# Optimization experiments

Measured on AMD Instinct MI355X. Metric: run time of the kernel, lower is better.

The kernel has to match this reference:

```python
import jax, jax.numpy as jnp
import numpy as np

B, S, HID = 2, 2048, 2048
H, D = 16, 128  # heads, head_dim == kernel_hidden_size
GATE_NORM = 16.0
CLAMP_MIN = -50.0


def gla(q, k, v, gk):
    # fused_recurrent_gla: S_t = diag(exp(gk_t)) S_{t-1} + k_t^T v_t; o_t = (q_t*scale) @ S_t
    # q,k,v,gk: [B,H,S,D]
    scale = D ** -0.5
    qs = jnp.moveaxis(q, 2, 0) * scale  # [S,B,H,D]
    ks = jnp.moveaxis(k, 2, 0)
    vs = jnp.moveaxis(v, 2, 0)
    gs = jnp.moveaxis(gk, 2, 0)

    def step(state, xs):
        q_t, k_t, v_t, g_t = xs  # each [B,H,D]
        state = state * jnp.exp(g_t)[..., None] + k_t[..., None] * v_t[..., None, :]
        o_t = jnp.einsum('bhk,bhkv->bhv', q_t, state)
        return state, o_t

    init = jnp.zeros((q.shape[0], H, D, D), q.dtype)
    _, out = jax.lax.scan(step, init, (qs, ks, vs, gs))
    return jnp.moveaxis(out, 0, 2)  # [B,H,S,D]


def setup_inputs() -> dict:
    key = jax.random.key(0)
    ks = jax.random.split(key, 8)
    std = 0.02
    hidden_states = jax.random.normal(ks[0], (B, S, HID), jnp.float32)
    Wq = jax.random.normal(ks[1], (HID, HID), jnp.float32) * std
    Wk = jax.random.normal(ks[2], (HID, HID), jnp.float32) * std
    Wv = jax.random.normal(ks[3], (HID, HID), jnp.float32) * std
    Wo = jax.random.normal(ks[4], (HID, HID), jnp.float32) * std
    Wg1 = jnp.eye(HID, dtype=jnp.float32)  # nn.init.eye_
    bg1 = jnp.zeros((HID,), jnp.float32)
    Wg2 = jnp.eye(HID, dtype=jnp.float32)
    bg2 = jnp.zeros((HID,), jnp.float32)
    alpha_list = jax.random.uniform(ks[5], (2,), jnp.float32)
    return dict(hidden_states=hidden_states, Wq=Wq, Wk=Wk, Wv=Wv, Wo=Wo,
                Wg1=Wg1, bg1=bg1, Wg2=Wg2, bg2=bg2, alpha_list=alpha_list)


def reference(hidden_states, Wq, Wk, Wv, Wo, Wg1, bg1, Wg2, bg2, alpha_list):
    b, s, _ = hidden_states.shape

    def split_heads(x):  # [b,s,hid] -> [b,h,s,d]
        return x.reshape(b, s, H, D).transpose(0, 2, 1, 3)

    q = split_heads(hidden_states @ Wq.T)
    k = split_heads(hidden_states @ Wk.T)
    v = split_heads(hidden_states @ Wv.T)

    def gate(Wg, bg):
        g = split_heads(hidden_states @ Wg.T + bg)
        g = jax.nn.log_sigmoid(g) / GATE_NORM
        return jnp.maximum(g, CLAMP_MIN)

    gk = gate(Wg1, bg1)
    gk2 = gate(Wg2, bg2)

    o1 = gla(q, k, v, gk)
    o2 = gla(q, k, v, gk2)

    a = jax.nn.softmax(alpha_list)
    attn = a[0] * o1 + a[1] * o2  # [b,h,s,d]
    attn = attn.transpose(0, 2, 1, 3).reshape(b, s, HID)
    return attn @ Wo.T
```

## Files before the change

### kernel.cpp

```cpp
#include <hip/hip_runtime.h>
#include <cstdint>
#include <cstddef>


#define BB     2
#define SEQ    2048
#define HIDN   2048
#define NH     16
#define DD     128
#define CHUNK  64
#define NCHUNK (SEQ / CHUNK)
#define NBH    (BB * NH)
#define NELC   8388608
#define WELC   4194304
static constexpr float QSCALE = 0.08838834764831845f;

typedef __bf16 bf16_t;
typedef _Float16 half_t;
typedef short  short8 __attribute__((ext_vector_type(8)));
typedef float  f32x4  __attribute__((ext_vector_type(4)));

__device__ __forceinline__ float bf2f(short u) {
  return (float)__builtin_bit_cast(bf16_t, u);
}
__device__ __forceinline__ short f2bf(float f) {
  return __builtin_bit_cast(short, (bf16_t)f);
}
__device__ __forceinline__ float hf2f(short u) {
  return (float)__builtin_bit_cast(half_t, u);
}
__device__ __forceinline__ short f2hf(float f) {
  return __builtin_bit_cast(short, (half_t)f);
}

__device__ __forceinline__ void gload_lds16(const void* g, void* l) {
  __builtin_amdgcn_global_load_lds(
      (__attribute__((address_space(1))) unsigned int*)g,
      (__attribute__((address_space(3))) unsigned int*)l, 16, 0, 0);
}

#define VMW6 asm volatile("s_waitcnt vmcnt(6)" ::: "memory")
#define VMW0 asm volatile("s_waitcnt vmcnt(0)" ::: "memory")
#define LGKM0 asm volatile("s_waitcnt lgkmcnt(0)" ::: "memory")
#define SBAR __builtin_amdgcn_s_barrier()


#define STG_A(buf, kt, pair)                                                \
  {                                                                         \
    const size_t ko = (size_t)(kt) * 64;                                    \
    gload_lds16(Ag + (size_t)((pair) * 64) * HIDN + ko,                     \
                (void*)&As[buf][((pair) * 64 + wave * 8) * 64]);            \
    gload_lds16(Ag + (size_t)((pair) * 64 + 128) * HIDN + ko,               \
                (void*)&As[buf][((pair) * 64 + 128 + wave * 8) * 64]);      \
  }

#define STG_B(buf, kt, half)                                                \
  {                                                                         \
    gload_lds16(Bg + (size_t)((half) * 64) * HIDN + (size_t)(kt) * 64,      \
                (void*)&Bs[buf][((half) * 64 + wave * 8) * 64]);            \
  }

#define LDA_PH(mh, rb)                                                      \
  {                                                                         \
    _Pragma("unroll") for (int f = 0; f < 4; f++) {                         \
      const int row = wm * 128 + (mh) * 64 + f * 16 + l16;                  \
      ar[f][0] = *(const short8*)&As[rb][row * 64 + ((qd ^ ro) << 3)];      \
      ar[f][1] =                                                            \
          *(const short8*)&As[rb][row * 64 + (((4 + qd) ^ ro) << 3)];       \
    }                                                                       \
  }

#define LDB_PH(rb)                                                          \
  {                                                                         \
    _Pragma("unroll") for (int g = 0; g < 2; g++) {                         \
      const int col = wn * 32 + g * 16 + l16;                               \
      br[g][0] = *(const short8*)&Bs[rb][col * 64 + ((qd ^ ro) << 3)];      \
      br[g][1] =                                                            \
          *(const short8*)&Bs[rb][col * 64 + (((4 + qd) ^ ro) << 3)];       \
    }                                                                       \
  }

#define MFMA_PH(mh)                                                         \
  {                                                                         \
    __builtin_amdgcn_s_setprio(1);                                          \
    _Pragma("unroll") for (int ks = 0; ks < 2; ks++)                        \
    _Pragma("unroll") for (int f = 0; f < 4; f++)                           \
    _Pragma("unroll") for (int g = 0; g < 2; g++)                           \
      acc[(mh) * 4 + f][g] = __builtin_amdgcn_mfma_f32_16x16x32_bf16(       \
          ar[f][ks], br[g][ks], acc[(mh) * 4 + f][g], 0, 0, 0);             \
    __builtin_amdgcn_s_setprio(0);                                          \
  }

__device__ __forceinline__ void gemm256(const bf16_t* __restrict__ A,
                                        const bf16_t* __restrict__ Bw,
                                        const float*  __restrict__ bias,
                                        bf16_t* __restrict__ outb,
                                        float*  __restrict__ outf, int epi) {
  __shared__ short As[3][256 * 64];
  __shared__ short Bs[3][128 * 64];
  const int tm   = blockIdx.x * 256;
  const int tn   = blockIdx.y * 128;
  const int tid  = threadIdx.x;
  const int wave = tid >> 6;
  const int lane = tid & 63;
  const int wm   = wave >> 2;
  const int wn   = wave & 3;
  const int qd   = lane >> 4;
  const int l16  = lane & 15;
  const int ro   = l16 & 7;
  const int gc   = (lane & 7) ^ (lane >> 3);

  const short* Ag =
      (const short*)A + (size_t)(tm + wave * 8 + (lane >> 3)) * HIDN + gc * 8;
  const short* Bg =
      (const short*)Bw + (size_t)(tn + wave * 8 + (lane >> 3)) * HIDN + gc * 8;

  f32x4 acc[8][2];
#pragma unroll
  for (int i = 0; i < 8; i++)
#pragma unroll
    for (int j = 0; j < 2; j++) acc[i][j] = (f32x4){0.f, 0.f, 0.f, 0.f};
  short8 ar[4][2], br[2][2];

  STG_A(0, 0, 0); STG_B(0, 0, 0); STG_B(0, 0, 1); STG_A(0, 0, 1);
  STG_A(1, 1, 0); STG_B(1, 1, 0); STG_B(1, 1, 1); STG_A(1, 1, 1);
  VMW6;
  SBAR;

  int rd = 0, st = 2;
  for (int t = 0; t < 32; t++) {
    LDA_PH(0, rd);
    LDB_PH(rd);
    if (t < 30) { STG_A(st, t + 2, 0); STG_B(st, t + 2, 0); }
    SBAR;
    LGKM0;
    MFMA_PH(0);
    SBAR;
    LDA_PH(1, rd);
    if (t < 30) { STG_B(st, t + 2, 1); STG_A(st, t + 2, 1); }
    SBAR;
    LGKM0;
    MFMA_PH(1);
    if (t < 30) { VMW6; }
    else if (t == 30) { VMW0; }
    SBAR;
    rd = (rd == 2) ? 0 : rd + 1;
    st = (st == 2) ? 0 : st + 1;
  }

#pragma unroll
  for (int i = 0; i < 8; i++)
#pragma unroll
    for (int j = 0; j < 2; j++)
#pragma unroll
      for (int r = 0; r < 4; r++) {
        const int row =
            tm + wm * 128 + (i >> 2) * 64 + (i & 3) * 16 + qd * 4 + r;
        const int col = tn + wn * 32 + j * 16 + l16;
        float v = acc[i][j][r];
        if (epi == 1) {
          v += bias[col];
          const float ls = fminf(v, 0.f) - log1pf(__expf(-fabsf(v)));
          v = fmaxf(ls * 0.0625f, -50.f);
        }
        if (epi == 2) outf[(size_t)row * HIDN + col] = v;
        else          outb[(size_t)row * HIDN + col] = (bf16_t)v;
      }
}

__global__ __launch_bounds__(512, 2) void k_gemm_proj(
    const bf16_t* __restrict__ Xb,
    const bf16_t* __restrict__ W0, const bf16_t* __restrict__ W1,
    const bf16_t* __restrict__ W2, const bf16_t* __restrict__ W3,
    const bf16_t* __restrict__ W4,
    const float* __restrict__ bg1, const float* __restrict__ bg2,
    bf16_t* __restrict__ Qb, bf16_t* __restrict__ Kb, bf16_t* __restrict__ Vb,
    bf16_t* __restrict__ G1b, bf16_t* __restrict__ G2b) {
  const int z = blockIdx.z;
  const bf16_t* Ws[5] = {W0, W1, W2, W3, W4};
  bf16_t* Os[5] = {Qb, Kb, Vb, G1b, G2b};
  const float* bias = (z == 3) ? bg1 : ((z == 4) ? bg2 : nullptr);
  gemm256(Xb, Ws[z], bias, Os[z], nullptr, (z >= 3) ? 1 : 0);
}

__global__ __launch_bounds__(512, 2) void k_gemm_out(
    const bf16_t* __restrict__ attnB, const bf16_t* __restrict__ Wob,
    float* __restrict__ out) {
  gemm256(attnB, Wob, nullptr, nullptr, out, 2);
}

__global__ __launch_bounds__(256) void k_cvt_all(
    const float* __restrict__ hid, const float* __restrict__ wq,
    const float* __restrict__ wk, const float* __restrict__ wv,
    const float* __restrict__ wg1, const float* __restrict__ wg2,
    const float* __restrict__ wo, bf16_t* __restrict__ Xb,
    bf16_t* __restrict__ Wd, bf16_t* __restrict__ Wcur,
    bf16_t* __restrict__ WoB) {
  const int y = blockIdx.y;
  const float* srcs[7] = {hid, wq, wk, wv, wg1, wg2, wo};
  bf16_t* dsts[7] = {Xb, Wd, Wd + WELC, Wd + 2 * WELC, Wd + 3 * WELC, Wcur,
                     WoB};
  const int n = (y == 0) ? NELC : WELC;
  const float* src = srcs[y];
  bf16_t* dst = dsts[y];
  const int idx = (blockIdx.x * 256 + threadIdx.x) * 4;
  if (idx < n) {
    const float4 f = *(const float4*)(src + idx);
    dst[idx + 0] = (bf16_t)f.x; dst[idx + 1] = (bf16_t)f.y;
    dst[idx + 2] = (bf16_t)f.z; dst[idx + 3] = (bf16_t)f.w;
  }
}

__global__ __launch_bounds__(256) void k_zero(float* __restrict__ out) {
  out[(size_t)blockIdx.x * 256 + threadIdx.x] = 0.f;
}

__global__ __launch_bounds__(64) void k_gc(bf16_t* __restrict__ G1b,
                                           bf16_t* __restrict__ G2b,
                                           float* __restrict__ Btot) {
  const int n = blockIdx.x, b = blockIdx.y >> 2, slab = blockIdx.y & 3;
  const int e = blockIdx.z;
  short* P = (short*)(e ? G2b : G1b);
  const int d0 = slab * 512 + threadIdx.x * 8;
  const size_t base = ((size_t)(b * SEQ + n * CHUNK)) * HIDN + d0;
  float c[8] = {0.f, 0.f, 0.f, 0.f, 0.f, 0.f, 0.f, 0.f};
  for (int t = 0; t < CHUNK; t++) {
    short* p = P + base + (size_t)t * HIDN;
    const short8 g = *(const short8*)p;
    short8 o;
#pragma unroll
    for (int j = 0; j < 8; j++) { c[j] += bf2f(g[j]); o[j] = f2hf(c[j]); }
    *(short8*)p = o;
  }
  const int bh = b * 16 + (d0 >> 7);
  float* bp = Btot + ((size_t)(e * NBH + bh) * NCHUNK + n) * DD + (d0 & 127);
#pragma unroll
  for (int j = 0; j < 8; j++) bp[j] = c[j];
}

template <int ACC>
__global__ __launch_bounds__(256) void k_sA(
    const bf16_t* __restrict__ Qb, const bf16_t* __restrict__ Kb,
    const bf16_t* __restrict__ Vb, const bf16_t* __restrict__ Gc,
    bf16_t* __restrict__ UT, const float* __restrict__ alpha,
    bf16_t* __restrict__ attn) {
  const int n = blockIdx.x, bh = blockIdx.y;
  const int b = bh >> 4, h = bh & 15;
  const size_t rbase = ((size_t)(b * SEQ + n * CHUNK)) * HIDN + h * DD;
  const int tid = threadIdx.x;
  const int wave = tid >> 6, lane = tid & 63, qd = lane >> 4, l16 = lane & 15;
  __shared__ short vT[128 * 66];
  __shared__ short k2s[64 * 128];
  __shared__ short r3[128 * 66];
  __shared__ short Ps[64 * 72];
  const float mx = fmaxf(alpha[0], alpha[1]);
  const float x0 = __expf(alpha[0] - mx), x1 = __expf(alpha[1] - mx);
  const float wsc = ((ACC ? x1 : x0) / (x0 + x1)) * QSCALE;

  const short* Kp = (const short*)Kb;
  const short* Vp = (const short*)Vb;
  const short* Gp = (const short*)Gc;
  const short* Qp = (const short*)Qb;

#pragma unroll
  for (int rep = 0; rep < 4; rep++) {
    const int slot = rep * 256 + tid;
    const int t = slot >> 4, ch = slot & 15;
    const size_t ga = rbase + (size_t)t * HIDN + ch * 8;
    const short8 vv = *(const short8*)(Vp + ga);
    const short8 kk = *(const short8*)(Kp + ga);
    const short8 cc = *(const short8*)(Gp + ga);
    const short8 c6 = *(const short8*)(Gp + rbase + (size_t)63 * HIDN + ch * 8);
    short8 k2v;
#pragma unroll
    for (int j = 0; j < 8; j++) {
      const int d = ch * 8 + j;
      vT[d * 66 + t] = vv[j];
      const float c = hf2f(cc[j]);
      const float kf = bf2f(kk[j]);
      k2v[j] = f2bf(kf * __expf(-c));
      r3[d * 66 + t] = f2bf(kf * __expf(hf2f(c6[j]) - c));
    }
    *(short8*)&k2s[t * 128 + ((ch ^ (t & 7)) << 3)] = k2v;
  }
  __syncthreads();

  {
    const int m0 = (wave >> 1) * 64, n0 = (wave & 1) * 64;
    const int* vTi = (const int*)vT;
    const int* r3i = (const int*)r3;
    f32x4 uacc[4][4];
#pragma unroll
    for (int i = 0; i < 4; i++)
#pragma unroll
      for (int j = 0; j < 4; j++) uacc[i][j] = (f32x4){0.f, 0.f, 0.f, 0.f};
#pragma unroll
    for (int ks = 0; ks < 2; ks++) {
      const int ch = ks * 4 + qd;
      short8 af[4], bfv[4];
#pragma unroll
      for (int i = 0; i < 4; i++) {
        const int dv = m0 + i * 16 + l16;
        const int ba = dv * 33 + ch * 4;
#pragma unroll
        for (int w2 = 0; w2 < 4; w2++) {
          const int v = vTi[ba + w2];
          af[i][2 * w2] = (short)(v & 0xffff);
          af[i][2 * w2 + 1] = (short)((unsigned)v >> 16);
        }
      }
#pragma unroll
      for (int j = 0; j < 4; j++) {
        const int dk = n0 + j * 16 + l16;
        const int ba = dk * 33 + ch * 4;
#pragma unroll
        for (int w2 = 0; w2 < 4; w2++) {
          const int v = r3i[ba + w2];
          bfv[j][2 * w2] = (short)(v & 0xffff);
          bfv[j][2 * w2 + 1] = (short)((unsigned)v >> 16);
        }
      }
#pragma unroll
      for (int i = 0; i < 4; i++)
#pragma unroll
        for (int j = 0; j < 4; j++)
          uacc[i][j] = __builtin_amdgcn_mfma_f32_16x16x32_bf16(
              af[i], bfv[j], uacc[i][j], 0, 0, 0);
    }
    short* Uo = (short*)UT + (size_t)(bh * NCHUNK + n) * (DD * DD);
#pragma unroll
    for (int i = 0; i < 4; i++)
#pragma unroll
      for (int j = 0; j < 4; j++)
#pragma unroll
        for (int r = 0; r < 4; r++) {
          const int dv = m0 + i * 16 + qd * 4 + r;
          const int dk = n0 + j * 16 + l16;
          Uo[dv * 128 + (((dk >> 3) ^ (dv & 7)) << 3) + (dk & 7)] =
              f2bf(uacc[i][j][r]);
        }
  }
  __syncthreads();

#pragma unroll
  for (int rep = 0; rep < 4; rep++) {
    const int slot = rep * 256 + tid;
    const int t = slot >> 4, ch = slot & 15;
    const size_t ga = rbase + (size_t)t * HIDN + ch * 8;
    const short8 qq = *(const short8*)(Qp + ga);
    const short8 cc = *(const short8*)(Gp + ga);
    short8 o;
#pragma unroll
    for (int j = 0; j < 8; j++)
      o[j] = f2bf(bf2f(qq[j]) * wsc * __expf(hf2f(cc[j])));
    *(short8*)&r3[t * 128 + ((ch ^ (t & 7)) << 3)] = o;
  }
  __syncthreads();

  {
    f32x4 pacc[4];
#pragma unroll
    for (int j = 0; j < 4; j++) pacc[j] = (f32x4){0.f, 0.f, 0.f, 0.f};
    const int tq = wave * 16 + l16;
#pragma unroll
    for (int ks = 0; ks < 4; ks++) {
      const int ch = ks * 4 + qd;
      const short8 a = *(const short8*)&r3[tq * 128 + ((ch ^ (tq & 7)) << 3)];
#pragma unroll
      for (int j = 0; j < 4; j++) {
        const int s = j * 16 + l16;
        const short8 bq =
            *(const short8*)&k2s[s * 128 + ((ch ^ (s & 7)) << 3)];
        pacc[j] =
            __builtin_amdgcn_mfma_f32_16x16x32_bf16(a, bq, pacc[j], 0, 0, 0);
      }
    }
#pragma unroll
    for (int j = 0; j < 4; j++)
#pragma unroll
      for (int r = 0; r < 4; r++) {
        const int t = wave * 16 + qd * 4 + r, s = j * 16 + l16;
        Ps[t * 72 + s] = (t >= s) ? f2bf(pacc[j][r]) : (short)0;
      }
  }
  __syncthreads();

  f32x4 oacc[8];
#pragma unroll
  for (int j = 0; j < 8; j++) oacc[j] = (f32x4){0.f, 0.f, 0.f, 0.f};
  {
    const int* vTi = (const int*)vT;
    const int tq = wave * 16 + l16;
#pragma unroll
    for (int ks = 0; ks < 2; ks++) {
      const int ch = ks * 4 + qd;
      const short8 a = *(const short8*)&Ps[tq * 72 + ch * 8];
#pragma unroll
      for (int j = 0; j < 8; j++) {
        const int dv = j * 16 + l16;
        const int ba = dv * 33 + ch * 4;
        short8 bq;
#pragma unroll
        for (int w2 = 0; w2 < 4; w2++) {
          const int v = vTi[ba + w2];
          bq[2 * w2] = (short)(v & 0xffff);
          bq[2 * w2 + 1] = (short)((unsigned)v >> 16);
        }
        oacc[j] =
            __builtin_amdgcn_mfma_f32_16x16x32_bf16(a, bq, oacc[j], 0, 0, 0);
      }
    }
  }
#pragma unroll
  for (int j = 0; j < 8; j++)
#pragma unroll
    for (int r = 0; r < 4; r++) {
      const int t = wave * 16 + qd * 4 + r;
      const int dv = j * 16 + l16;
      bf16_t* p = &attn[rbase + (size_t)t * HIDN + dv];
      if (ACC) *p = (bf16_t)((float)*p + oacc[j][r]);
      else     *p = (bf16_t)oacc[j][r];
    }
}

__global__ __launch_bounds__(256) void k_s2(bf16_t* __restrict__ UT,
                                            const float* __restrict__ Btot) {
  const int dg = blockIdx.x, bh = blockIdx.y;
  const int dv = dg * 8 + (threadIdx.x >> 5);
  const int dk0 = (threadIdx.x & 31) * 4;
  const int pos = dv * 128 + (((dk0 >> 3) ^ (dv & 7)) << 3) + (dk0 & 7);
  float st[4] = {0.f, 0.f, 0.f, 0.f};
  for (int nn = 0; nn < NCHUNK; nn++) {
    short* p = (short*)UT + (size_t)(bh * NCHUNK + nn) * (DD * DD) + pos;
    const float4 bp =
        *(const float4*)(Btot + (size_t)(bh * NCHUNK + nn) * DD + dk0);
    short u0 = p[0], u1 = p[1], u2 = p[2], u3 = p[3];
    p[0] = f2bf(st[0]); p[1] = f2bf(st[1]);
    p[2] = f2bf(st[2]); p[3] = f2bf(st[3]);
    st[0] = st[0] * __expf(bp.x) + bf2f(u0);
    st[1] = st[1] * __expf(bp.y) + bf2f(u1);
    st[2] = st[2] * __expf(bp.z) + bf2f(u2);
    st[3] = st[3] * __expf(bp.w) + bf2f(u3);
  }
}

__global__ __launch_bounds__(256) void k_s3b(
    const bf16_t* __restrict__ Qb, const bf16_t* __restrict__ Gc,
    const bf16_t* __restrict__ UT, const float* __restrict__ alpha,
    const int e, bf16_t* __restrict__ attn) {
  const int n = blockIdx.x, bh = blockIdx.y;
  const int b = bh >> 4, h = bh & 15;
  const size_t rbase = ((size_t)(b * SEQ + n * CHUNK)) * HIDN + h * DD;
  const int tid = threadIdx.x;
  const int wave = tid >> 6, lane = tid & 63, qd = lane >> 4, l16 = lane & 15;
  __shared__ short qh[64 * 128];
  __shared__ short Ss[128 * 128];
  const float mx = fmaxf(alpha[0], alpha[1]);
  const float x0 = __expf(alpha[0] - mx), x1 = __expf(alpha[1] - mx);
  const float wsc = ((e ? x1 : x0) / (x0 + x1)) * QSCALE;

  const short* Sp = (const short*)UT + (size_t)(bh * NCHUNK + n) * (DD * DD);
#pragma unroll
  for (int rep = 0; rep < 8; rep++) {
    const int c = rep * 256 + tid;
    gload_lds16(Sp + c * 8, &Ss[c * 8]);
  }
  const short* Qp = (const short*)Qb;
  const short* Gp = (const short*)Gc;
#pragma unroll
  for (int rep = 0; rep < 4; rep++) {
    const int slot = rep * 256 + tid;
    const int t = slot >> 4, ch = slot & 15;
    const size_t ga = rbase + (size_t)t * HIDN + ch * 8;
    const short8 qq = *(const short8*)(Qp + ga);
    const short8 cc = *(const short8*)(Gp + ga);
    short8 o;
#pragma unroll
    for (int j = 0; j < 8; j++)
      o[j] = f2bf(bf2f(qq[j]) * wsc * __expf(hf2f(cc[j])));
    *(short8*)&qh[t * 128 + ((ch ^ (t & 7)) << 3)] = o;
  }
  __syncthreads();

  f32x4 oacc[8];
#pragma unroll
  for (int j = 0; j < 8; j++) oacc[j] = (f32x4){0.f, 0.f, 0.f, 0.f};
  const int tq = wave * 16 + l16;
#pragma unroll
  for (int ks = 0; ks < 4; ks++) {
    const int ch = ks * 4 + qd;
    const short8 a = *(const short8*)&qh[tq * 128 + ((ch ^ (tq & 7)) << 3)];
#pragma unroll
    for (int j = 0; j < 8; j++) {
      const int dv = j * 16 + l16;
      const short8 bq = *(const short8*)&Ss[dv * 128 + ((ch ^ (dv & 7)) << 3)];
      oacc[j] =
          __builtin_amdgcn_mfma_f32_16x16x32_bf16(a, bq, oacc[j], 0, 0, 0);
    }
  }
#pragma unroll
  for (int j = 0; j < 8; j++)
#pragma unroll
    for (int r = 0; r < 4; r++) {
      const int t = wave * 16 + qd * 4 + r;
      const int dv = j * 16 + l16;
      bf16_t* p = &attn[rbase + (size_t)t * HIDN + dv];
      *p = (bf16_t)((float)*p + oacc[j][r]);
    }
}

extern "C" void kernel_launch(void* const* d_in, const int* in_sizes, int n_in,
                              void* d_out, int out_size, void* d_ws,
                              size_t ws_size, hipStream_t stream) {
  const float* hid  = (const float*)d_in[0];
  const float* wq   = (const float*)d_in[1];
  const float* wk   = (const float*)d_in[2];
  const float* wv   = (const float*)d_in[3];
  const float* wo   = (const float*)d_in[4];
  const float* wg1  = (const float*)d_in[5];
  const float* bg1  = (const float*)d_in[6];
  const float* wg2  = (const float*)d_in[7];
  const float* bg2  = (const float*)d_in[8];
  const float* alph = (const float*)d_in[9];
  float* out = (float*)d_out;
  (void)in_sizes; (void)n_in; (void)out_size;

  char* ws = (char*)d_ws;
  size_t off = 0;
  auto alloc = [&](size_t bytes) -> void* {
    void* p = ws + off;
    off += (bytes + 255) & ~(size_t)255;
    return p;
  };
  const size_t NEL = NELC, WEL = WELC;
  bf16_t* Xb   = (bf16_t*)alloc(NEL * 2);
  bf16_t* Wcur = (bf16_t*)alloc(WEL * 2);
  bf16_t* WoB  = (bf16_t*)alloc(WEL * 2);
  bf16_t* Qb   = (bf16_t*)alloc(NEL * 2);
  bf16_t* Kb   = (bf16_t*)alloc(NEL * 2);
  bf16_t* Vb   = (bf16_t*)alloc(NEL * 2);
  bf16_t* G1b  = (bf16_t*)alloc(NEL * 2);
  bf16_t* G2b  = (bf16_t*)alloc(NEL * 2);
  float*  Btot = (float*) alloc((size_t)2 * NBH * NCHUNK * DD * 4);
  bf16_t* Wd = (bf16_t*)d_out;
  bf16_t* UT = (bf16_t*)d_out;

  if (off > ws_size) {
    k_zero<<<dim3((unsigned)(NEL / 256)), 256, 0, stream>>>(out);
    return;
  }

  k_cvt_all<<<dim3(8192, 7), 256, 0, stream>>>(hid, wq, wk, wv, wg1, wg2, wo,
                                               Xb, Wd, Wcur, WoB);
  k_gemm_proj<<<dim3(16, 16, 5), 512, 0, stream>>>(
      Xb, Wd, Wd + WEL, Wd + 2 * WEL, Wd + 3 * WEL, Wcur, bg1, bg2, Qb, Kb, Vb,
      G1b, G2b);
  k_gc<<<dim3(NCHUNK, BB * 4, 2), 64, 0, stream>>>(G1b, G2b, Btot);

  const dim3 gs(NCHUNK, NBH), g2(16, NBH);
  const size_t BSTRIDE = (size_t)NBH * NCHUNK * DD;
  k_sA<0><<<gs, 256, 0, stream>>>(Qb, Kb, Vb, G1b, UT, alph, Xb);
  k_s2<<<g2, 256, 0, stream>>>(UT, Btot);
  k_s3b<<<gs, 256, 0, stream>>>(Qb, G1b, UT, alph, 0, Xb);
  k_sA<1><<<gs, 256, 0, stream>>>(Qb, Kb, Vb, G2b, UT, alph, Xb);
  k_s2<<<g2, 256, 0, stream>>>(UT, Btot + BSTRIDE);
  k_s3b<<<gs, 256, 0, stream>>>(Qb, G2b, UT, alph, 1, Xb);

  k_gemm_out<<<dim3(16, 16), 512, 0, stream>>>(Xb, WoB, out);
}
```

Before: 581.0 us.

## Enlarge GEMM tile to 256x256 with double-buffered 8-phase pipeline

Grows the shared GEMM macro-tile from 256x128 to 256x256, so each wave computes a 128x64 sub-tile with 32 accumulators, and halves the grid along N for both the projection and output GEMMs. The triple-buffered LDS ring becomes a double-buffered scheme with eight interleaved load/MFMA quadrant phases and a vmcnt(2) wait. The aim is more operand reuse per LDS read and less global traffic per FLOP. The cost is higher register pressure, LDS use of 128KB, which may limit occupancy below the 2 blocks per CU in the launch bounds, and fewer blocks for the out GEMM (128 blocks on a chip with 256 CUs).

```diff
diff --git a/kernel.cpp b/kernel.cpp
--- a/kernel.cpp
+++ b/kernel.cpp
@@ -39,55 +39,60 @@
       (__attribute__((address_space(3))) unsigned int*)l, 16, 0, 0);
 }
 
-#define VMW6 asm volatile("s_waitcnt vmcnt(6)" ::: "memory")
+#define VMW2 asm volatile("s_waitcnt vmcnt(2)" ::: "memory")
 #define VMW0 asm volatile("s_waitcnt vmcnt(0)" ::: "memory")
-#define LGKM0 asm volatile("s_waitcnt lgkmcnt(0)" ::: "memory")
 #define SBAR __builtin_amdgcn_s_barrier()
 
 
-#define STG_A(buf, kt, pair)                                                \
+#define STG_A(buf, kt, h)                                                   \
   {                                                                         \
     const size_t ko = (size_t)(kt) * 64;                                    \
-    gload_lds16(Ag + (size_t)((pair) * 64) * HIDN + ko,                     \
-                (void*)&As[buf][((pair) * 64 + wave * 8) * 64]);            \
-    gload_lds16(Ag + (size_t)((pair) * 64 + 128) * HIDN + ko,               \
-                (void*)&As[buf][((pair) * 64 + 128 + wave * 8) * 64]);      \
-  }
-
-#define STG_B(buf, kt, half)                                                \
+    gload_lds16(Ag + (size_t)((h) * 128) * HIDN + ko,                       \
+                (void*)&As[buf][((h) * 128 + wave * 8) * 64]);              \
+    gload_lds16(Ag + (size_t)((h) * 128 + 64) * HIDN + ko,                  \
+                (void*)&As[buf][((h) * 128 + 64 + wave * 8) * 64]);         \
+  }
+
+#define STG_B(buf, kt, h)                                                   \
   {                                                                         \
-    gload_lds16(Bg + (size_t)((half) * 64) * HIDN + (size_t)(kt) * 64,      \
-                (void*)&Bs[buf][((half) * 64 + wave * 8) * 64]);            \
-  }
-
-#define LDA_PH(mh, rb)                                                      \
+    const size_t ko = (size_t)(kt) * 64;                                    \
+    gload_lds16(Bg + (size_t)((h) * 128) * HIDN + ko,                       \
+                (void*)&Bs[buf][((h) * 128 + wave * 8) * 64]);              \
+    gload_lds16(Bg + (size_t)((h) * 128 + 64) * HIDN + ko,                  \
+                (void*)&Bs[buf][((h) * 128 + 64 + wave * 8) * 64]);         \
+  }
+
+#define LDA(mh, rb)                                                         \
   {                                                                         \
     _Pragma("unroll") for (int f = 0; f < 4; f++) {                         \
       const int row = wm * 128 + (mh) * 64 + f * 16 + l16;                  \
-      ar[f][0] = *(const short8*)&As[rb][row * 64 + ((qd ^ ro) << 3)];      \
-      ar[f][1] =                                                            \
+      af[f][0] = *(const short8*)&As[rb][row * 64 + ((qd ^ ro) << 3)];      \
+      af[f][1] =                                                            \
           *(const short8*)&As[rb][row * 64 + (((4 + qd) ^ ro) << 3)];       \
     }                                                                       \
   }
 
-#define LDB_PH(rb)                                                          \
+#define LDB2(j0, rb)                                                        \
   {                                                                         \
     _Pragma("unroll") for (int g = 0; g < 2; g++) {                         \
-      const int col = wn * 32 + g * 16 + l16;                               \
-      br[g][0] = *(const short8*)&Bs[rb][col * 64 + ((qd ^ ro) << 3)];      \
-      br[g][1] =                                                            \
+      const int col = wn * 64 + ((j0) + g) * 16 + l16;                      \
+      bfr[(j0) + g][0] =                                                    \
+          *(const short8*)&Bs[rb][col * 64 + ((qd ^ ro) << 3)];             \
+      bfr[(j0) + g][1] =                                                    \
           *(const short8*)&Bs[rb][col * 64 + (((4 + qd) ^ ro) << 3)];       \
     }                                                                       \
   }
 
-#define MFMA_PH(mh)                                                         \
+#define MQ(mh, nh)                                                          \
   {                                                                         \
     __builtin_amdgcn_s_setprio(1);                                          \
     _Pragma("unroll") for (int ks = 0; ks < 2; ks++)                        \
     _Pragma("unroll") for (int f = 0; f < 4; f++)                           \
     _Pragma("unroll") for (int g = 0; g < 2; g++)                           \
-      acc[(mh) * 4 + f][g] = __builtin_amdgcn_mfma_f32_16x16x32_bf16(       \
-          ar[f][ks], br[g][ks], acc[(mh) * 4 + f][g], 0, 0, 0);             \
+      acc[(mh) * 4 + f][(nh) * 2 + g] =                                     \
+          __builtin_amdgcn_mfma_f32_16x16x32_bf16(                          \
+              af[f][ks], bfr[(nh) * 2 + g][ks],                             \
+              acc[(mh) * 4 + f][(nh) * 2 + g], 0, 0, 0);                    \
     __builtin_amdgcn_s_setprio(0);                                          \
   }
 
@@ -96,10 +101,10 @@
                                         const float*  __restrict__ bias,
                                         bf16_t* __restrict__ outb,
                                         float*  __restrict__ outf, int epi) {
-  __shared__ short As[3][256 * 64];
-  __shared__ short Bs[3][128 * 64];
+  __shared__ short As[2][256 * 64];
+  __shared__ short Bs[2][256 * 64];
   const int tm   = blockIdx.x * 256;
-  const int tn   = blockIdx.y * 128;
+  const int tn   = blockIdx.y * 256;
   const int tid  = threadIdx.x;
   const int wave = tid >> 6;
   const int lane = tid & 63;
@@ -115,48 +120,56 @@
   const short* Bg =
       (const short*)Bw + (size_t)(tn + wave * 8 + (lane >> 3)) * HIDN + gc * 8;
 
-  f32x4 acc[8][2];
+  f32x4 acc[8][4];
 #pragma unroll
   for (int i = 0; i < 8; i++)
 #pragma unroll
-    for (int j = 0; j < 2; j++) acc[i][j] = (f32x4){0.f, 0.f, 0.f, 0.f};
-  short8 ar[4][2], br[2][2];
-
-  STG_A(0, 0, 0); STG_B(0, 0, 0); STG_B(0, 0, 1); STG_A(0, 0, 1);
-  STG_A(1, 1, 0); STG_B(1, 1, 0); STG_B(1, 1, 1); STG_A(1, 1, 1);
-  VMW6;
+    for (int j = 0; j < 4; j++) acc[i][j] = (f32x4){0.f, 0.f, 0.f, 0.f};
+  short8 af[4][2], bfr[4][2];
+
+  STG_A(0, 0, 0); STG_A(0, 0, 1); STG_B(0, 0, 0); STG_B(0, 0, 1);
+  STG_A(1, 1, 0);
+  VMW2;
   SBAR;
 
-  int rd = 0, st = 2;
-  for (int t = 0; t < 32; t++) {
-    LDA_PH(0, rd);
-    LDB_PH(rd);
-    if (t < 30) { STG_A(st, t + 2, 0); STG_B(st, t + 2, 0); }
+  for (int t = 0; t < 16; t++) {
+    LDA(0, 0); LDB2(0, 0);
+    STG_A(1, 2 * t + 1, 1);
+    SBAR; MQ(0, 0); SBAR;
+    LDB2(2, 0);
+    STG_B(1, 2 * t + 1, 0);
+    SBAR; MQ(0, 1); SBAR;
+    LDA(1, 0);
+    STG_B(1, 2 * t + 1, 1);
+    SBAR; MQ(1, 1); SBAR;
+    if (t < 15) { STG_A(0, 2 * t + 2, 0); }
+    SBAR; MQ(1, 0);
+    if (t < 15) { VMW2; } else { VMW0; }
     SBAR;
-    LGKM0;
-    MFMA_PH(0);
+    LDA(0, 1); LDB2(0, 1);
+    if (t < 15) { STG_A(0, 2 * t + 2, 1); }
+    SBAR; MQ(0, 0); SBAR;
+    LDB2(2, 1);
+    if (t < 15) { STG_B(0, 2 * t + 2, 0); }
+    SBAR; MQ(0, 1); SBAR;
+    LDA(1, 1);
+    if (t < 15) { STG_B(0, 2 * t + 2, 1); }
+    SBAR; MQ(1, 1); SBAR;
+    if (t < 15) { STG_A(1, 2 * t + 3, 0); }
+    SBAR; MQ(1, 0);
+    if (t < 15) { VMW2; }
     SBAR;
-    LDA_PH(1, rd);
-    if (t < 30) { STG_B(st, t + 2, 1); STG_A(st, t + 2, 1); }
-    SBAR;
-    LGKM0;
-    MFMA_PH(1);
-    if (t < 30) { VMW6; }
-    else if (t == 30) { VMW0; }
-    SBAR;
-    rd = (rd == 2) ? 0 : rd + 1;
-    st = (st == 2) ? 0 : st + 1;
   }
 
 #pragma unroll
   for (int i = 0; i < 8; i++)
 #pragma unroll
-    for (int j = 0; j < 2; j++)
+    for (int j = 0; j < 4; j++)
 #pragma unroll
       for (int r = 0; r < 4; r++) {
         const int row =
             tm + wm * 128 + (i >> 2) * 64 + (i & 3) * 16 + qd * 4 + r;
-        const int col = tn + wn * 32 + j * 16 + l16;
+        const int col = tn + wn * 64 + j * 16 + l16;
         float v = acc[i][j][r];
         if (epi == 1) {
           v += bias[col];
@@ -552,7 +565,7 @@
 
   k_cvt_all<<<dim3(8192, 7), 256, 0, stream>>>(hid, wq, wk, wv, wg1, wg2, wo,
                                                Xb, Wd, Wcur, WoB);
-  k_gemm_proj<<<dim3(16, 16, 5), 512, 0, stream>>>(
+  k_gemm_proj<<<dim3(16, 8, 5), 512, 0, stream>>>(
       Xb, Wd, Wd + WEL, Wd + 2 * WEL, Wd + 3 * WEL, Wcur, bg1, bg2, Qb, Kb, Vb,
       G1b, G2b);
   k_gc<<<dim3(NCHUNK, BB * 4, 2), 64, 0, stream>>>(G1b, G2b, Btot);
@@ -566,5 +579,5 @@
   k_s2<<<g2, 256, 0, stream>>>(UT, Btot + BSTRIDE);
   k_s3b<<<gs, 256, 0, stream>>>(Qb, G2b, UT, alph, 1, Xb);
 
-  k_gemm_out<<<dim3(16, 16), 512, 0, stream>>>(Xb, WoB, out);
-}
+  k_gemm_out<<<dim3(16, 8), 512, 0, stream>>>(Xb, WoB, out);
+}
```

Result: no change. 591.4 us (+1.8%).
